# Optimization experiments

Hardware: AMD Instinct MI355X
Metric: run time of the kernel (lower is better)

The kernel has to match this reference:

```python
import jax, jax.numpy as jnp
import numpy as np

# Sylo forward (symmetry='psd', coupling=None, bias=True, remove_diagonal=True)
# Template: T[o,c] = L[o,c] @ L[o,c]^T  (psd => R == L, no coupling)
# crosshair_dot(A,B)[i,j] = sum_k P[k,j] + sum_k P[i,k] - P[i,j], P = A*B
# crosshair_similarity sums crosshair_dot over in_channels; then +bias, zero diagonal.

N, C_IN, C_OUT, DIM, RANK = 8, 4, 64, 512, 4


def setup_inputs() -> dict:
    key = jax.random.key(0)
    kx, kl, kb = jax.random.split(key, 3)
    X = jax.random.normal(kx, (N, C_IN, DIM, DIM), dtype=jnp.float32)
    weight_L = jax.random.normal(kl, (C_OUT, C_IN, DIM, RANK), dtype=jnp.float32) * 0.05
    bias = jax.random.normal(kb, (C_OUT,), dtype=jnp.float32) * 0.05
    return {"X": X, "weight_L": weight_L, "bias": bias}


def reference(X, weight_L, bias):
    # templates: (C_out, C_in, H, W)
    T = jnp.einsum('ochr,ocwr->ochw', weight_L, weight_L)
    # P summed over in_channels: (N, C_out, H, W)
    P = jnp.einsum('nchw,ochw->nohw', X, T)
    # column sums (sum over rows h) and row sums (sum over cols w), summed over c
    col_sums = jnp.einsum('nchw,ochw->now', X, T)  # (N, C_out, W)
    row_sums = jnp.einsum('nchw,ochw->noh', X, T)  # (N, C_out, H)
    out = row_sums[..., :, None] + col_sums[..., None, :] - P
    out = out + bias[:, None, None]
    # delete diagonal
    mask = 1.0 - jnp.eye(out.shape[-1], dtype=out.dtype)
    return out * mask
```

## Files before the change

kernel.cpp:

```cpp
#include <hip/hip_runtime.h>


#define DIMS 512
#define CIN 4
#define COUT 64
#define NB 8
#define RANKS 4

typedef float f32x4 __attribute__((ext_vector_type(4)));

#define LPK_ELEMS (CIN * DIMS * COUT * RANKS)
#define SUMS_ELEMS (NB * COUT * DIMS)

__global__ __launch_bounds__(256) void pack_L(const float* __restrict__ L,
                                              float* __restrict__ Lpk) {
    int idx = blockIdx.x * 256 + threadIdx.x;
    int oc = idx & 255;
    int k  = (idx >> 8) & 511;
    int c  = idx >> 17;
    int o = oc >> 2, r = oc & 3;
    Lpk[idx] = L[((o * CIN + c) * DIMS + k) * RANKS + r];
}

#define XPAD 68

__global__ __launch_bounds__(256) void sums_kernel(const float* __restrict__ X,
                                                   const float* __restrict__ Lpk,
                                                   float* __restrict__ sums) {
    const int mode = blockIdx.y;
    const int n    = blockIdx.x >> 5;
    const int d0   = (blockIdx.x & 31) << 4;
    const int t    = threadIdx.x;
    const int lane = t & 63;
    const int drow = (t >> 6) << 2;

    __shared__ float Xsm[16 * XPAD];
    const float4* __restrict__ Lpk4 = (const float4*)Lpk;

    float rsacc[4] = {0.f, 0.f, 0.f, 0.f};

    for (int c = 0; c < CIN; ++c) {
        float acc[4][4];
#pragma unroll
        for (int i = 0; i < 4; ++i)
#pragma unroll
            for (int j = 0; j < 4; ++j) acc[i][j] = 0.f;

        const float* __restrict__ Xc = X + (size_t)(n * CIN + c) * DIMS * DIMS;

        for (int k0 = 0; k0 < DIMS; k0 += 64) {
            __syncthreads();
            if (mode == 0) {
                int kk = t & 63, dd = t >> 6;
#pragma unroll
                for (int j = 0; j < 4; ++j)
                    Xsm[(dd + 4 * j) * XPAD + kk] = Xc[(d0 + dd + 4 * j) * DIMS + k0 + kk];
            } else {
                int dd = t & 15, kk0 = t >> 4;
#pragma unroll
                for (int j = 0; j < 4; ++j)
                    Xsm[dd * XPAD + kk0 + 16 * j] = Xc[(k0 + kk0 + 16 * j) * DIMS + d0 + dd];
            }
            __syncthreads();

#pragma unroll 2
            for (int k = 0; k < 64; k += 4) {
                float4 lv0 = Lpk4[(c * DIMS + k0 + k + 0) * 64 + lane];
                float4 lv1 = Lpk4[(c * DIMS + k0 + k + 1) * 64 + lane];
                float4 lv2 = Lpk4[(c * DIMS + k0 + k + 2) * 64 + lane];
                float4 lv3 = Lpk4[(c * DIMS + k0 + k + 3) * 64 + lane];
#pragma unroll
                for (int i = 0; i < 4; ++i) {
                    float4 xv = *(const float4*)&Xsm[(drow + i) * XPAD + k];
                    acc[i][0] += xv.x * lv0.x + xv.y * lv1.x + xv.z * lv2.x + xv.w * lv3.x;
                    acc[i][1] += xv.x * lv0.y + xv.y * lv1.y + xv.z * lv2.y + xv.w * lv3.y;
                    acc[i][2] += xv.x * lv0.z + xv.y * lv1.z + xv.z * lv2.z + xv.w * lv3.z;
                    acc[i][3] += xv.x * lv0.w + xv.y * lv1.w + xv.z * lv2.w + xv.w * lv3.w;
                }
            }
        }
#pragma unroll
        for (int i = 0; i < 4; ++i) {
            float4 lf = Lpk4[(c * DIMS + d0 + drow + i) * 64 + lane];
            rsacc[i] += lf.x * acc[i][0] + lf.y * acc[i][1] + lf.z * acc[i][2] + lf.w * acc[i][3];
        }
    }

    float* __restrict__ dst = sums + mode * SUMS_ELEMS;
#pragma unroll
    for (int i = 0; i < 4; ++i)
        dst[(n * COUT + lane) * DIMS + d0 + drow + i] = rsacc[i];
}

__global__ __launch_bounds__(256) void final_kernel(const float* __restrict__ X,
                                                    const float* __restrict__ L,
                                                    const float* __restrict__ bias,
                                                    const float* __restrict__ sums,
                                                    float* __restrict__ out) {
    const int o    = blockIdx.x;
    const int tile = blockIdx.y;
    const int h0   = (tile & 7) << 6;
    const int w0   = (tile >> 3) << 6;
    const int t    = threadIdx.x;

    __shared__ float Tsm[CIN * 64 * 64];
    __shared__ float Lhs[CIN * 64 * 5];
    __shared__ float Lws[CIN * 64 * 5];

    for (int idx = t; idx < 2 * CIN * 64 * RANKS; idx += 256) {
        int side = idx >> 10;
        int rem  = idx & 1023;
        int c    = rem >> 8;
        int d    = (rem >> 2) & 63;
        int r    = rem & 3;
        int base = side ? w0 : h0;
        float v  = L[((o * CIN + c) * DIMS + base + d) * RANKS + r];
        (side ? Lws : Lhs)[(c * 64 + d) * 5 + r] = v;
    }
    __syncthreads();

    {
        int ww = t & 63;
        int hb = t >> 6;
        for (int c = 0; c < CIN; ++c) {
#pragma unroll
            for (int i = 0; i < 16; ++i) {
                int hh = hb + 4 * i;
                float s = 0.f;
#pragma unroll
                for (int r = 0; r < RANKS; ++r)
                    s += Lhs[(c * 64 + hh) * 5 + r] * Lws[(c * 64 + ww) * 5 + r];
                Tsm[c * 4096 + hh * 64 + ww] = s;
            }
        }
    }
    __syncthreads();

    const float4* __restrict__ X4   = (const float4*)X;
    const float4* __restrict__ Tsm4 = (const float4*)Tsm;
    f32x4* __restrict__ out4        = (f32x4*)out;
    const float* __restrict__ rs    = sums;
    const float* __restrict__ cs    = sums + SUMS_ELEMS;
    const float b = bias[o];

    const int ww4   = t & 15;
    const int hbase = t >> 4;

    for (int n = 0; n < NB; ++n) {
#pragma unroll
        for (int i = 0; i < 4; ++i) {
            int hh = hbase + 16 * i;
            int hg = h0 + hh;
            float4 p = {0.f, 0.f, 0.f, 0.f};
#pragma unroll
            for (int c = 0; c < CIN; ++c) {
                float4 xv = X4[((size_t)((n * CIN + c) * DIMS + hg) * DIMS + w0) / 4 + ww4];
                float4 tv = Tsm4[(c * 4096 + hh * 64) / 4 + ww4];
                p.x += xv.x * tv.x;
                p.y += xv.y * tv.y;
                p.z += xv.z * tv.z;
                p.w += xv.w * tv.w;
            }
            float rv = rs[(n * COUT + o) * DIMS + hg] + b;
            float4 cv = *(const float4*)&cs[(n * COUT + o) * DIMS + w0 + 4 * ww4];
            f32x4 ov;
            ov.x = rv + cv.x - p.x;
            ov.y = rv + cv.y - p.y;
            ov.z = rv + cv.z - p.z;
            ov.w = rv + cv.w - p.w;
            int wg = w0 + 4 * ww4;
            if (hg == wg)     ov.x = 0.f;
            if (hg == wg + 1) ov.y = 0.f;
            if (hg == wg + 2) ov.z = 0.f;
            if (hg == wg + 3) ov.w = 0.f;
            __builtin_nontemporal_store(ov,
                &out4[((size_t)((n * COUT + o) * DIMS + hg) * DIMS + w0) / 4 + ww4]);
        }
    }
}

extern "C" void kernel_launch(void* const* d_in, const int* in_sizes, int n_in,
                              void* d_out, int out_size, void* d_ws, size_t ws_size,
                              hipStream_t stream) {
    (void)in_sizes; (void)n_in; (void)out_size; (void)ws_size;
    const float* X    = (const float*)d_in[0];
    const float* L    = (const float*)d_in[1];
    const float* bias = (const float*)d_in[2];
    float* out = (float*)d_out;
    float* ws  = (float*)d_ws;

    float* Lpk  = ws;
    float* sums = ws + LPK_ELEMS;

    pack_L<<<LPK_ELEMS / 256, 256, 0, stream>>>(L, Lpk);
    sums_kernel<<<dim3(256, 2), 256, 0, stream>>>(X, Lpk, sums);
    final_kernel<<<dim3(64, 64), 256, 0, stream>>>(X, L, bias, sums, out);
}
```

Before: 771.1 us.

## Register-resident templates, two output channels per block, wider sums blocks

The final kernel now uses 32x32 tiles and computes the template entries directly in registers, dropping the large 64KB shared-memory template buffer. Each block handles two output channels, so every X load is reused for both. The sums kernel moves to 512 threads, each handling 2 rows instead of 4, which raises parallelism and lowers per-thread register pressure. In exchange there are more blocks and more redundant L loads per tile, plus extra bias and row/column-sum loads.

New measurement: 824.1 us. +6.9%, slower.

```diff
diff --git a/kernel.cpp b/kernel.cpp
--- a/kernel.cpp
+++ b/kernel.cpp
@@ -24,25 +24,25 @@
 
 #define XPAD 68
 
-__global__ __launch_bounds__(256) void sums_kernel(const float* __restrict__ X,
-                                                   const float* __restrict__ Lpk,
-                                                   float* __restrict__ sums) {
+__global__ __launch_bounds__(512, 4) void sums_kernel(const float* __restrict__ X,
+                                                      const float* __restrict__ Lpk,
+                                                      float* __restrict__ sums) {
     const int mode = blockIdx.y;
     const int n    = blockIdx.x >> 5;
     const int d0   = (blockIdx.x & 31) << 4;
     const int t    = threadIdx.x;
     const int lane = t & 63;
-    const int drow = (t >> 6) << 2;
+    const int drow = (t >> 6) << 1;
 
     __shared__ float Xsm[16 * XPAD];
     const float4* __restrict__ Lpk4 = (const float4*)Lpk;
 
-    float rsacc[4] = {0.f, 0.f, 0.f, 0.f};
+    float rsacc[2] = {0.f, 0.f};
 
     for (int c = 0; c < CIN; ++c) {
-        float acc[4][4];
-#pragma unroll
-        for (int i = 0; i < 4; ++i)
+        float acc[2][4];
+#pragma unroll
+        for (int i = 0; i < 2; ++i)
 #pragma unroll
             for (int j = 0; j < 4; ++j) acc[i][j] = 0.f;
 
@@ -53,13 +53,13 @@
             if (mode == 0) {
                 int kk = t & 63, dd = t >> 6;
 #pragma unroll
-                for (int j = 0; j < 4; ++j)
-                    Xsm[(dd + 4 * j) * XPAD + kk] = Xc[(d0 + dd + 4 * j) * DIMS + k0 + kk];
+                for (int j = 0; j < 2; ++j)
+                    Xsm[(dd + 8 * j) * XPAD + kk] = Xc[(d0 + dd + 8 * j) * DIMS + k0 + kk];
             } else {
                 int dd = t & 15, kk0 = t >> 4;
 #pragma unroll
-                for (int j = 0; j < 4; ++j)
-                    Xsm[dd * XPAD + kk0 + 16 * j] = Xc[(k0 + kk0 + 16 * j) * DIMS + d0 + dd];
+                for (int j = 0; j < 2; ++j)
+                    Xsm[dd * XPAD + kk0 + 32 * j] = Xc[(k0 + kk0 + 32 * j) * DIMS + d0 + dd];
             }
             __syncthreads();
 
@@ -70,7 +70,7 @@
                 float4 lv2 = Lpk4[(c * DIMS + k0 + k + 2) * 64 + lane];
                 float4 lv3 = Lpk4[(c * DIMS + k0 + k + 3) * 64 + lane];
 #pragma unroll
-                for (int i = 0; i < 4; ++i) {
+                for (int i = 0; i < 2; ++i) {
                     float4 xv = *(const float4*)&Xsm[(drow + i) * XPAD + k];
                     acc[i][0] += xv.x * lv0.x + xv.y * lv1.x + xv.z * lv2.x + xv.w * lv3.x;
                     acc[i][1] += xv.x * lv0.y + xv.y * lv1.y + xv.z * lv2.y + xv.w * lv3.y;
@@ -80,7 +80,7 @@
             }
         }
 #pragma unroll
-        for (int i = 0; i < 4; ++i) {
+        for (int i = 0; i < 2; ++i) {
             float4 lf = Lpk4[(c * DIMS + d0 + drow + i) * 64 + lane];
             rsacc[i] += lf.x * acc[i][0] + lf.y * acc[i][1] + lf.z * acc[i][2] + lf.w * acc[i][3];
         }
@@ -88,93 +88,120 @@
 
     float* __restrict__ dst = sums + mode * SUMS_ELEMS;
 #pragma unroll
-    for (int i = 0; i < 4; ++i)
+    for (int i = 0; i < 2; ++i)
         dst[(n * COUT + lane) * DIMS + d0 + drow + i] = rsacc[i];
 }
 
-__global__ __launch_bounds__(256) void final_kernel(const float* __restrict__ X,
-                                                    const float* __restrict__ L,
-                                                    const float* __restrict__ bias,
-                                                    const float* __restrict__ sums,
-                                                    float* __restrict__ out) {
-    const int o    = blockIdx.x;
+#define OPB 2
+
+__global__ __launch_bounds__(256, 4) void final_kernel(const float* __restrict__ X,
+                                                       const float* __restrict__ L,
+                                                       const float* __restrict__ bias,
+                                                       const float* __restrict__ sums,
+                                                       float* __restrict__ out) {
+    const int o0   = blockIdx.x * OPB;
     const int tile = blockIdx.y;
-    const int h0   = (tile & 7) << 6;
-    const int w0   = (tile >> 3) << 6;
+    const int h0   = (tile & 15) << 5;
+    const int w0   = (tile >> 4) << 5;
     const int t    = threadIdx.x;
-
-    __shared__ float Tsm[CIN * 64 * 64];
-    __shared__ float Lhs[CIN * 64 * 5];
-    __shared__ float Lws[CIN * 64 * 5];
-
-    for (int idx = t; idx < 2 * CIN * 64 * RANKS; idx += 256) {
-        int side = idx >> 10;
-        int rem  = idx & 1023;
-        int c    = rem >> 8;
-        int d    = (rem >> 2) & 63;
-        int r    = rem & 3;
-        int base = side ? w0 : h0;
-        float v  = L[((o * CIN + c) * DIMS + base + d) * RANKS + r];
-        (side ? Lws : Lhs)[(c * 64 + d) * 5 + r] = v;
+    const int ww4  = t & 7;
+    const int hh   = t >> 3;
+
+    __shared__ float Lhs[OPB * CIN * 32 * RANKS];
+    __shared__ float Lws[OPB * CIN * 32 * RANKS];
+
+    {
+        const float4* __restrict__ L4 = (const float4*)L;
+        float4* __restrict__ LhsV = (float4*)Lhs;
+        float4* __restrict__ LwsV = (float4*)Lws;
+        for (int idx = t; idx < 2 * OPB * CIN * 32; idx += 256) {
+            int side = idx >> 8;
+            int rem  = idx & 255;
+            int o2   = rem >> 7;
+            int c    = (rem >> 5) & 3;
+            int d    = rem & 31;
+            int base = side ? w0 : h0;
+            float4 v = L4[((o0 + o2) * CIN + c) * DIMS + base + d];
+            (side ? LwsV : LhsV)[rem] = v;
+        }
     }
     __syncthreads();
 
+    float4 Tr[OPB][CIN];
     {
-        int ww = t & 63;
-        int hb = t >> 6;
+        const float4* __restrict__ Lh4 = (const float4*)Lhs;
+        const float4* __restrict__ Lw4 = (const float4*)Lws;
+#pragma unroll
+        for (int o2 = 0; o2 < OPB; ++o2)
+#pragma unroll
+            for (int c = 0; c < CIN; ++c) {
+                float4 lh  = Lh4[(o2 * CIN + c) * 32 + hh];
+                float4 wv0 = Lw4[(o2 * CIN + c) * 32 + 4 * ww4 + 0];
+                float4 wv1 = Lw4[(o2 * CIN + c) * 32 + 4 * ww4 + 1];
+                float4 wv2 = Lw4[(o2 * CIN + c) * 32 + 4 * ww4 + 2];
+                float4 wv3 = Lw4[(o2 * CIN + c) * 32 + 4 * ww4 + 3];
+                Tr[o2][c].x = lh.x * wv0.x + lh.y * wv0.y + lh.z * wv0.z + lh.w * wv0.w;
+                Tr[o2][c].y = lh.x * wv1.x + lh.y * wv1.y + lh.z * wv1.z + lh.w * wv1.w;
+                Tr[o2][c].z = lh.x * wv2.x + lh.y * wv2.y + lh.z * wv2.z + lh.w * wv2.w;
+                Tr[o2][c].w = lh.x * wv3.x + lh.y * wv3.y + lh.z * wv3.z + lh.w * wv3.w;
+            }
+    }
+
+    const float4* __restrict__ X4 = (const float4*)X;
+    f32x4* __restrict__ out4      = (f32x4*)out;
+    const float* __restrict__ rs  = sums;
+    const float* __restrict__ cs  = sums + SUMS_ELEMS;
+    const float b0 = bias[o0];
+    const float b1 = bias[o0 + 1];
+
+    const int hg  = h0 + hh;
+    const int wgb = w0 + 4 * ww4;
+    const size_t xoff = (size_t)hg * (DIMS / 4) + (w0 >> 2) + ww4;
+
+    for (int n = 0; n < NB; ++n) {
+        float4 p0 = {0.f, 0.f, 0.f, 0.f};
+        float4 p1 = {0.f, 0.f, 0.f, 0.f};
+#pragma unroll
         for (int c = 0; c < CIN; ++c) {
-#pragma unroll
-            for (int i = 0; i < 16; ++i) {
-                int hh = hb + 4 * i;
-                float s = 0.f;
-#pragma unroll
-                for (int r = 0; r < RANKS; ++r)
-                    s += Lhs[(c * 64 + hh) * 5 + r] * Lws[(c * 64 + ww) * 5 + r];
-                Tsm[c * 4096 + hh * 64 + ww] = s;
-            }
-        }
-    }
-    __syncthreads();
-
-    const float4* __restrict__ X4   = (const float4*)X;
-    const float4* __restrict__ Tsm4 = (const float4*)Tsm;
-    f32x4* __restrict__ out4        = (f32x4*)out;
-    const float* __restrict__ rs    = sums;
-    const float* __restrict__ cs    = sums + SUMS_ELEMS;
-    const float b = bias[o];
-
-    const int ww4   = t & 15;
-    const int hbase = t >> 4;
-
-    for (int n = 0; n < NB; ++n) {
-#pragma unroll
-        for (int i = 0; i < 4; ++i) {
-            int hh = hbase + 16 * i;
-            int hg = h0 + hh;
-            float4 p = {0.f, 0.f, 0.f, 0.f};
-#pragma unroll
-            for (int c = 0; c < CIN; ++c) {
-                float4 xv = X4[((size_t)((n * CIN + c) * DIMS + hg) * DIMS + w0) / 4 + ww4];
-                float4 tv = Tsm4[(c * 4096 + hh * 64) / 4 + ww4];
-                p.x += xv.x * tv.x;
-                p.y += xv.y * tv.y;
-                p.z += xv.z * tv.z;
-                p.w += xv.w * tv.w;
-            }
-            float rv = rs[(n * COUT + o) * DIMS + hg] + b;
-            float4 cv = *(const float4*)&cs[(n * COUT + o) * DIMS + w0 + 4 * ww4];
+            float4 xv = X4[(size_t)(n * CIN + c) * (DIMS * DIMS / 4) + xoff];
+            p0.x += xv.x * Tr[0][c].x;
+            p0.y += xv.y * Tr[0][c].y;
+            p0.z += xv.z * Tr[0][c].z;
+            p0.w += xv.w * Tr[0][c].w;
+            p1.x += xv.x * Tr[1][c].x;
+            p1.y += xv.y * Tr[1][c].y;
+            p1.z += xv.z * Tr[1][c].z;
+            p1.w += xv.w * Tr[1][c].w;
+        }
+        {
+            float  rv = rs[(n * COUT + o0) * DIMS + hg] + b0;
+            float4 cv = *(const float4*)&cs[(n * COUT + o0) * DIMS + wgb];
             f32x4 ov;
-            ov.x = rv + cv.x - p.x;
-            ov.y = rv + cv.y - p.y;
-            ov.z = rv + cv.z - p.z;
-            ov.w = rv + cv.w - p.w;
-            int wg = w0 + 4 * ww4;
-            if (hg == wg)     ov.x = 0.f;
-            if (hg == wg + 1) ov.y = 0.f;
-            if (hg == wg + 2) ov.z = 0.f;
-            if (hg == wg + 3) ov.w = 0.f;
+            ov.x = rv + cv.x - p0.x;
+            ov.y = rv + cv.y - p0.y;
+            ov.z = rv + cv.z - p0.z;
+            ov.w = rv + cv.w - p0.w;
+            if (hg == wgb)     ov.x = 0.f;
+            if (hg == wgb + 1) ov.y = 0.f;
+            if (hg == wgb + 2) ov.z = 0.f;
+            if (hg == wgb + 3) ov.w = 0.f;
             __builtin_nontemporal_store(ov,
-                &out4[((size_t)((n * COUT + o) * DIMS + hg) * DIMS + w0) / 4 + ww4]);
+                &out4[((size_t)(n * COUT + o0) * DIMS + hg) * (DIMS / 4) + (w0 >> 2) + ww4]);
+        }
+        {
+            float  rv = rs[(n * COUT + o0 + 1) * DIMS + hg] + b1;
+            float4 cv = *(const float4*)&cs[(n * COUT + o0 + 1) * DIMS + wgb];
+            f32x4 ov;
+            ov.x = rv + cv.x - p1.x;
+            ov.y = rv + cv.y - p1.y;
+            ov.z = rv + cv.z - p1.z;
+            ov.w = rv + cv.w - p1.w;
+            if (hg == wgb)     ov.x = 0.f;
+            if (hg == wgb + 1) ov.y = 0.f;
+            if (hg == wgb + 2) ov.z = 0.f;
+            if (hg == wgb + 3) ov.w = 0.f;
+            __builtin_nontemporal_store(ov,
+                &out4[((size_t)(n * COUT + o0 + 1) * DIMS + hg) * (DIMS / 4) + (w0 >> 2) + ww4]);
         }
     }
 }
@@ -193,6 +220,6 @@
     float* sums = ws + LPK_ELEMS;
 
     pack_L<<<LPK_ELEMS / 256, 256, 0, stream>>>(L, Lpk);
-    sums_kernel<<<dim3(256, 2), 256, 0, stream>>>(X, Lpk, sums);
-    final_kernel<<<dim3(64, 64), 256, 0, stream>>>(X, L, bias, sums, out);
-}
+    sums_kernel<<<dim3(256, 2), 512, 0, stream>>>(X, Lpk, sums);
+    final_kernel<<<dim3(COUT / OPB, 256), 256, 0, stream>>>(X, L, bias, sums, out);
+}
```
